# Performance work log

Hardware: AMD Instinct MI355X
Metric: run time of the kernel (lower is better)

## Reference

```python
import jax, jax.numpy as jnp
import numpy as np

N, B, D, Q = 32, 36, 2048, 1024  # batch, objects, v_dim, q_dim


def setup_inputs() -> dict:
    key = jax.random.key(0)
    ks = jax.random.split(key, 6)
    sc = 0.02  # small init so ReLU chains stay well-scaled
    return {
        "v": jax.random.normal(ks[0], (N, B, D), jnp.float32),
        "q": jax.random.normal(ks[1], (N, Q), jnp.float32),
        "W1": jax.random.normal(ks[2], (D, D), jnp.float32) * sc,
        "b1": jnp.zeros((D,), jnp.float32),
        "W2": jax.random.normal(ks[3], (D, D), jnp.float32) * sc,
        "b2": jnp.zeros((D,), jnp.float32),
        "W3": jax.random.normal(ks[4], (Q, D), jnp.float32) * sc,
        "b3": jnp.zeros((D,), jnp.float32),
    }


def reference(v, q, W1, b1, W2, b2, W3, b3):
    # FCNet = ReLU(Linear(.)) with weight-norm folded, dropout=0 (eval).
    # Original calls linear3 twice (linear4 unused bug), so q_emb == q_emb2.
    qe = jax.nn.relu(q @ W3 + b3)  # (N, D)
    # pairs[n,i,j] = v[n,i]*qe[n] + v[n,j]*qe[n]  -> (N, B, B, D)
    pairs = (v[:, :, None, :] + v[:, None, :, :]) * qe[:, None, None, :]
    h = jax.nn.relu(jnp.einsum('nijd,de->nije', pairs, W1) + b1)  # linear1
    x = jnp.sum(h, axis=2)  # sum over j relations -> (N, B, D)
    return jax.nn.relu(x @ W2 + b2)  # linear2
```

## Files before the change

kernel.cpp:

```cpp
#include <hip/hip_runtime.h>
#include <stdint.h>

#define N_BATCH 32
#define B_OBJ   36
#define D_DIM   2048
#define Q_DIM   1024

typedef __bf16 bf16x8 __attribute__((ext_vector_type(8)));
typedef float  f32x4  __attribute__((ext_vector_type(4)));

__device__ __forceinline__ uint16_t f2bf(float f) {
    uint32_t u = __builtin_bit_cast(uint32_t, f);
    uint32_t r = (u + 0x7FFFu + ((u >> 16) & 1u)) >> 16;
    return (uint16_t)r;
}

__device__ __forceinline__ void gld_lds16(const void* g, void* l) {
    __builtin_amdgcn_global_load_lds(
        (const __attribute__((address_space(1))) uint32_t*)g,
        (__attribute__((address_space(3))) uint32_t*)l, 16, 0, 0);
}

__global__ __launch_bounds__(256) void transpose_all(
    const float* __restrict__ W1, const float* __restrict__ W2,
    uint16_t* __restrict__ W1t, uint16_t* __restrict__ W2t) {
    __shared__ float tile[64][65];
    int gy = blockIdx.y;
    const float* W; uint16_t* Wt; int k0;
    if (gy < 32) { W = W1; Wt = W1t; k0 = gy * 64; }
    else         { W = W2; Wt = W2t; k0 = (gy - 32) * 64; }
    int n0 = blockIdx.x * 64;
    int t = threadIdx.x;
    {
        int r = t >> 4, c = (t & 15) * 4;
#pragma unroll
        for (int p = 0; p < 4; ++p)
            *(float4*)&tile[r + p * 16][c] =
                *(const float4*)&W[(size_t)(k0 + r + p * 16) * 2048 + n0 + c];
    }
    __syncthreads();
    {
        int n = t >> 2, kb = (t & 3) * 16;
#pragma unroll
        for (int g4 = 0; g4 < 4; ++g4) {
            int k = kb + g4 * 4;
            ushort4 o;
            o.x = f2bf(tile[k][n]);     o.y = f2bf(tile[k + 1][n]);
            o.z = f2bf(tile[k + 2][n]); o.w = f2bf(tile[k + 3][n]);
            *(ushort4*)&Wt[(size_t)(n0 + n) * 2048 + k0 + k] = o;
        }
    }
}

__global__ __launch_bounds__(256) void qe_f32(
    const float* __restrict__ q, const float* __restrict__ W3,
    float* __restrict__ qpart) {
    __shared__ float qs[128][32];
    int t = threadIdx.x;
    int e0 = blockIdx.x * 64;
    int kbase = blockIdx.y * 128;
    {
        int nn = t >> 3, kg = (t & 7) * 16;
#pragma unroll
        for (int p = 0; p < 4; ++p) {
            float4 f = *(const float4*)&q[(size_t)nn * Q_DIM + kbase + kg + p * 4];
            qs[kg + p * 4 + 0][nn] = f.x; qs[kg + p * 4 + 1][nn] = f.y;
            qs[kg + p * 4 + 2][nn] = f.z; qs[kg + p * 4 + 3][nn] = f.w;
        }
    }
    __syncthreads();
    int n = t >> 3, e8 = (t & 7) * 8;
    float acc[8] = {};
#pragma unroll 4
    for (int k = 0; k < 128; ++k) {
        float qv = qs[k][n];
        float4 wa = *(const float4*)&W3[(size_t)(kbase + k) * D_DIM + e0 + e8];
        float4 wb = *(const float4*)&W3[(size_t)(kbase + k) * D_DIM + e0 + e8 + 4];
        acc[0] += qv * wa.x; acc[1] += qv * wa.y; acc[2] += qv * wa.z; acc[3] += qv * wa.w;
        acc[4] += qv * wb.x; acc[5] += qv * wb.y; acc[6] += qv * wb.z; acc[7] += qv * wb.w;
    }
    float* dst = qpart + (size_t)blockIdx.y * 32 * D_DIM + (size_t)n * D_DIM + e0 + e8;
    *(float4*)dst = *(float4*)&acc[0];
    *(float4*)(dst + 4) = *(float4*)&acc[4];
}

__global__ __launch_bounds__(256) void qe_makeu(
    const float* __restrict__ qpart, const float* __restrict__ b3,
    const float* __restrict__ v, uint16_t* __restrict__ u) {
    int n = blockIdx.y;
    int c4 = blockIdx.x * 256 + threadIdx.x;
    const float4* p = (const float4*)qpart;
    size_t base = (size_t)n * 512 + c4;
    float4 s = p[base];
#pragma unroll
    for (int z = 1; z < 8; ++z) {
        float4 sz = p[(size_t)z * 16384 + base];
        s.x += sz.x; s.y += sz.y; s.z += sz.z; s.w += sz.w;
    }
    float4 b = ((const float4*)b3)[c4];
    float4 qe;
    qe.x = fmaxf(s.x + b.x, 0.f); qe.y = fmaxf(s.y + b.y, 0.f);
    qe.z = fmaxf(s.z + b.z, 0.f); qe.w = fmaxf(s.w + b.w, 0.f);
    const float4* v4 = (const float4*)v + (size_t)n * B_OBJ * 512 + c4;
    ushort4* u4 = (ushort4*)u + (size_t)n * B_OBJ * 512 + c4;
#pragma unroll 4
    for (int i = 0; i < B_OBJ; ++i) {
        float4 vv = v4[(size_t)i * 512];
        ushort4 o;
        o.x = f2bf(vv.x * qe.x); o.y = f2bf(vv.y * qe.y);
        o.z = f2bf(vv.z * qe.z); o.w = f2bf(vv.w * qe.w);
        u4[(size_t)i * 512] = o;
    }
}

__global__ __launch_bounds__(256) void gemm_ks(
    const uint16_t* __restrict__ A,
    const uint16_t* __restrict__ Bt,
    float* __restrict__ Yp) {
    __shared__ __align__(16) uint16_t sm[24576];
    int t = threadIdx.x, lane = t & 63, wave = t >> 6;
    int l15 = lane & 15, quad = lane >> 4;
    int wr = wave >> 1, wc = wave & 1;
    int n0 = blockIdx.x * 64, m0 = blockIdx.y * 128, kz = blockIdx.z;
    const uint16_t* Ab = A  + (size_t)m0 * D_DIM + kz * 1024;
    const uint16_t* Bb = Bt + (size_t)n0 * D_DIM + kz * 1024;

    const uint16_t* gp[6]; uint16_t* lp[6]; int ofs[6];
#pragma unroll
    for (int c = 0; c < 6; ++c) {
        int r = wave + 4 * c;
        int row16 = lane >> 2, kin = (lane & 3) * 8;
        if (r < 16) {
            int h = r >> 3, g = r & 7;
            gp[c] = Ab + (size_t)(g * 16 + row16) * D_DIM + h * 32 + kin;
            lp[c] = sm + h * 4096 + g * 512;
            ofs[c] = 8192;
        } else {
            int rb = r - 16, h = rb >> 2, g = rb & 3;
            gp[c] = Bb + (size_t)(g * 16 + row16) * D_DIM + h * 32 + kin;
            lp[c] = sm + 16384 + h * 2048 + g * 512;
            ofs[c] = 4096;
        }
    }

    f32x4 acc[4][2] = {};

#pragma unroll
    for (int c = 0; c < 6; ++c) gld_lds16(gp[c], lp[c]);

    for (int it = 0; it < 16; ++it) {
        int buf = it & 1;
        __syncthreads();
        if (it < 15) {
            int nxt = buf ^ 1;
#pragma unroll
            for (int c = 0; c < 6; ++c)
                gld_lds16(gp[c] + (it + 1) * 64, lp[c] + nxt * ofs[c]);
        }
#pragma unroll
        for (int s = 0; s < 2; ++s) {
            bf16x8 af[4], bfr[2];
#pragma unroll
            for (int i = 0; i < 4; ++i)
                af[i] = *(const bf16x8*)(sm + buf * 8192 + s * 4096 +
                                         (wr * 64 + i * 16 + l15) * 32 + quad * 8);
#pragma unroll
            for (int j = 0; j < 2; ++j)
                bfr[j] = *(const bf16x8*)(sm + 16384 + buf * 4096 + s * 2048 +
                                          (wc * 32 + j * 16 + l15) * 32 + quad * 8);
#pragma unroll
            for (int i = 0; i < 4; ++i)
#pragma unroll
                for (int j = 0; j < 2; ++j)
                    acc[i][j] = __builtin_amdgcn_mfma_f32_16x16x32_bf16(af[i], bfr[j], acc[i][j], 0, 0, 0);
        }
    }

    float* Y = Yp + (size_t)kz * 1152 * D_DIM;
#pragma unroll
    for (int i = 0; i < 4; ++i)
#pragma unroll
        for (int j = 0; j < 2; ++j) {
            int col = n0 + wc * 32 + j * 16 + l15;
#pragma unroll
            for (int r = 0; r < 4; ++r)
                Y[(size_t)(m0 + wr * 64 + i * 16 + quad * 4 + r) * D_DIM + col] = acc[i][j][r];
        }
}

__global__ __launch_bounds__(256) void pairsum_red(
    const float* __restrict__ Yp, const float* __restrict__ b1,
    uint16_t* __restrict__ X) {
    int n = blockIdx.y;
    int d = blockIdx.x * 256 + threadIdx.x;
    const float* y0 = Yp + (size_t)(n * B_OBJ) * D_DIM + d;
    const float* y1 = y0 + (size_t)1152 * D_DIM;
    float z[B_OBJ];
#pragma unroll
    for (int j = 0; j < B_OBJ; ++j)
        z[j] = y0[(size_t)j * D_DIM] + y1[(size_t)j * D_DIM];
    float b = b1[d];
    uint16_t* xb = X + (size_t)(n * B_OBJ) * D_DIM + d;
#pragma unroll
    for (int i = 0; i < B_OBJ; ++i) {
        float zi = z[i] + b;
        float s = 0.f;
#pragma unroll
        for (int j = 0; j < B_OBJ; ++j) s += fmaxf(zi + z[j], 0.f);
        xb[(size_t)i * D_DIM] = f2bf(s);
    }
}

__global__ __launch_bounds__(256) void reduce_out(
    const float* __restrict__ Op, const float* __restrict__ b2,
    float* __restrict__ out) {
    int i = blockIdx.x * 256 + threadIdx.x;
    const float4* p = (const float4*)Op;
    float4 a = p[i], b = p[589824 + i];
    float4 bb = ((const float4*)b2)[i & 511];
    float4 o;
    o.x = fmaxf(a.x + b.x + bb.x, 0.f);
    o.y = fmaxf(a.y + b.y + bb.y, 0.f);
    o.z = fmaxf(a.z + b.z + bb.z, 0.f);
    o.w = fmaxf(a.w + b.w + bb.w, 0.f);
    ((float4*)out)[i] = o;
}

extern "C" void kernel_launch(void* const* d_in, const int* in_sizes, int n_in,
                              void* d_out, int out_size, void* d_ws, size_t ws_size,
                              hipStream_t stream) {
    const float* v  = (const float*)d_in[0];
    const float* q  = (const float*)d_in[1];
    const float* W1 = (const float*)d_in[2];
    const float* b1 = (const float*)d_in[3];
    const float* W2 = (const float*)d_in[4];
    const float* b2 = (const float*)d_in[5];
    const float* W3 = (const float*)d_in[6];
    const float* b3 = (const float*)d_in[7];
    float* out = (float*)d_out;

    char* ws = (char*)d_ws;
    uint16_t* W1t   = (uint16_t*)(ws + 0);
    uint16_t* W2t   = (uint16_t*)(ws + 8388608);
    uint16_t* u     = (uint16_t*)(ws + 16777216);
    float*    qpart = (float*)   (ws + 21495808);
    uint16_t* x     = (uint16_t*)(ws + 23592960);
    float*    Yp    = (float*)   (ws + 28311552);
    float*    Op    = Yp;

    transpose_all<<<dim3(32, 64), 256, 0, stream>>>(W1, W2, W1t, W2t);

    qe_f32<<<dim3(32, 8), 256, 0, stream>>>(q, W3, qpart);
    qe_makeu<<<dim3(2, N_BATCH), 256, 0, stream>>>(qpart, b3, v, u);

    gemm_ks<<<dim3(32, 9, 2), 256, 0, stream>>>(u, W1t, Yp);
    pairsum_red<<<dim3(8, N_BATCH), 256, 0, stream>>>(Yp, b1, x);

    gemm_ks<<<dim3(32, 9, 2), 256, 0, stream>>>(x, W2t, Op);
    reduce_out<<<2304, 256, 0, stream>>>(Op, b2, out);
}
```

Before: 185.8 us.

## Fuse pairwise-relu reduction and bias epilogues into full-K GEMM with 32x32 MFMA

Result: slower. 190.3 us (+2.4%).

```diff
diff --git a/kernel.cpp b/kernel.cpp
--- a/kernel.cpp
+++ b/kernel.cpp
@@ -6,8 +6,9 @@
 #define D_DIM   2048
 #define Q_DIM   1024
 
-typedef __bf16 bf16x8 __attribute__((ext_vector_type(8)));
-typedef float  f32x4  __attribute__((ext_vector_type(4)));
+typedef __bf16 bf16x8  __attribute__((ext_vector_type(8)));
+typedef float  f32x4   __attribute__((ext_vector_type(4)));
+typedef float  f32x16  __attribute__((ext_vector_type(16)));
 
 __device__ __forceinline__ uint16_t f2bf(float f) {
     uint32_t u = __builtin_bit_cast(uint32_t, f);
@@ -113,117 +114,108 @@
     }
 }
 
-__global__ __launch_bounds__(256) void gemm_ks(
+__global__ __launch_bounds__(128) void gemm_fused(
     const uint16_t* __restrict__ A,
     const uint16_t* __restrict__ Bt,
-    float* __restrict__ Yp) {
-    __shared__ __align__(16) uint16_t sm[24576];
+    const float* __restrict__ bias,
+    void* __restrict__ Cv,
+    int mode) {
+    __shared__ __align__(16) uint16_t sm[20480];
+    float* yt = (float*)sm;
+
     int t = threadIdx.x, lane = t & 63, wave = t >> 6;
-    int l15 = lane & 15, quad = lane >> 4;
-    int wr = wave >> 1, wc = wave & 1;
-    int n0 = blockIdx.x * 64, m0 = blockIdx.y * 128, kz = blockIdx.z;
-    const uint16_t* Ab = A  + (size_t)m0 * D_DIM + kz * 1024;
-    const uint16_t* Bb = Bt + (size_t)n0 * D_DIM + kz * 1024;
-
-    const uint16_t* gp[6]; uint16_t* lp[6]; int ofs[6];
-#pragma unroll
-    for (int c = 0; c < 6; ++c) {
-        int r = wave + 4 * c;
+    int l31 = lane & 31, khalf = lane >> 5;
+    int bg = blockIdx.y;
+    int n0 = blockIdx.x * 64;
+    const uint16_t* Ab = A + (size_t)bg * 72 * D_DIM;
+
+    const uint16_t* gp[10]; uint16_t* lp[10]; int bufstep[10];
+    {
         int row16 = lane >> 2, kin = (lane & 3) * 8;
-        if (r < 16) {
-            int h = r >> 3, g = r & 7;
-            gp[c] = Ab + (size_t)(g * 16 + row16) * D_DIM + h * 32 + kin;
-            lp[c] = sm + h * 4096 + g * 512;
-            ofs[c] = 8192;
-        } else {
-            int rb = r - 16, h = rb >> 2, g = rb & 3;
-            gp[c] = Bb + (size_t)(g * 16 + row16) * D_DIM + h * 32 + kin;
-            lp[c] = sm + 16384 + h * 2048 + g * 512;
-            ofs[c] = 4096;
-        }
-    }
-
-    f32x4 acc[4][2] = {};
-
-#pragma unroll
-    for (int c = 0; c < 6; ++c) gld_lds16(gp[c], lp[c]);
-
-    for (int it = 0; it < 16; ++it) {
+#pragma unroll
+        for (int c = 0; c < 10; ++c) {
+            int r = wave * 10 + c;
+            if (r < 12) {
+                int h = r / 6, g = r % 6;
+                gp[c] = Ab + (size_t)(g * 16 + row16) * D_DIM + h * 32 + kin;
+                lp[c] = sm + h * 3072 + g * 512;
+                bufstep[c] = 6144;
+            } else {
+                int rb = r - 12, h = rb >> 2, g = rb & 3;
+                gp[c] = Bt + (size_t)(n0 + g * 16 + row16) * D_DIM + h * 32 + kin;
+                lp[c] = sm + 12288 + h * 2048 + g * 512;
+                bufstep[c] = 4096;
+            }
+        }
+    }
+
+    f32x16 acc[3] = {};
+
+#pragma unroll
+    for (int c = 0; c < 10; ++c) gld_lds16(gp[c], lp[c]);
+
+    for (int it = 0; it < 32; ++it) {
         int buf = it & 1;
         __syncthreads();
-        if (it < 15) {
+        if (it < 31) {
             int nxt = buf ^ 1;
 #pragma unroll
-            for (int c = 0; c < 6; ++c)
-                gld_lds16(gp[c] + (it + 1) * 64, lp[c] + nxt * ofs[c]);
-        }
-#pragma unroll
-        for (int s = 0; s < 2; ++s) {
-            bf16x8 af[4], bfr[2];
-#pragma unroll
-            for (int i = 0; i < 4; ++i)
-                af[i] = *(const bf16x8*)(sm + buf * 8192 + s * 4096 +
-                                         (wr * 64 + i * 16 + l15) * 32 + quad * 8);
-#pragma unroll
-            for (int j = 0; j < 2; ++j)
-                bfr[j] = *(const bf16x8*)(sm + 16384 + buf * 4096 + s * 2048 +
-                                          (wc * 32 + j * 16 + l15) * 32 + quad * 8);
-#pragma unroll
-            for (int i = 0; i < 4; ++i)
-#pragma unroll
-                for (int j = 0; j < 2; ++j)
-                    acc[i][j] = __builtin_amdgcn_mfma_f32_16x16x32_bf16(af[i], bfr[j], acc[i][j], 0, 0, 0);
-        }
-    }
-
-    float* Y = Yp + (size_t)kz * 1152 * D_DIM;
-#pragma unroll
-    for (int i = 0; i < 4; ++i)
-#pragma unroll
-        for (int j = 0; j < 2; ++j) {
-            int col = n0 + wc * 32 + j * 16 + l15;
-#pragma unroll
-            for (int r = 0; r < 4; ++r)
-                Y[(size_t)(m0 + wr * 64 + i * 16 + quad * 4 + r) * D_DIM + col] = acc[i][j][r];
-        }
-}
-
-__global__ __launch_bounds__(256) void pairsum_red(
-    const float* __restrict__ Yp, const float* __restrict__ b1,
-    uint16_t* __restrict__ X) {
-    int n = blockIdx.y;
-    int d = blockIdx.x * 256 + threadIdx.x;
-    const float* y0 = Yp + (size_t)(n * B_OBJ) * D_DIM + d;
-    const float* y1 = y0 + (size_t)1152 * D_DIM;
-    float z[B_OBJ];
-#pragma unroll
-    for (int j = 0; j < B_OBJ; ++j)
-        z[j] = y0[(size_t)j * D_DIM] + y1[(size_t)j * D_DIM];
-    float b = b1[d];
-    uint16_t* xb = X + (size_t)(n * B_OBJ) * D_DIM + d;
-#pragma unroll
-    for (int i = 0; i < B_OBJ; ++i) {
-        float zi = z[i] + b;
-        float s = 0.f;
-#pragma unroll
-        for (int j = 0; j < B_OBJ; ++j) s += fmaxf(zi + z[j], 0.f);
-        xb[(size_t)i * D_DIM] = f2bf(s);
-    }
-}
-
-__global__ __launch_bounds__(256) void reduce_out(
-    const float* __restrict__ Op, const float* __restrict__ b2,
-    float* __restrict__ out) {
-    int i = blockIdx.x * 256 + threadIdx.x;
-    const float4* p = (const float4*)Op;
-    float4 a = p[i], b = p[589824 + i];
-    float4 bb = ((const float4*)b2)[i & 511];
-    float4 o;
-    o.x = fmaxf(a.x + b.x + bb.x, 0.f);
-    o.y = fmaxf(a.y + b.y + bb.y, 0.f);
-    o.z = fmaxf(a.z + b.z + bb.z, 0.f);
-    o.w = fmaxf(a.w + b.w + bb.w, 0.f);
-    ((float4*)out)[i] = o;
+            for (int c = 0; c < 10; ++c)
+                gld_lds16(gp[c] + (size_t)(it + 1) * 64, lp[c] + nxt * bufstep[c]);
+        }
+#pragma unroll
+        for (int s = 0; s < 4; ++s) {
+            int h = s >> 1, kin = (s & 1) * 16 + khalf * 8;
+            bf16x8 bfr = *(const bf16x8*)(sm + 12288 + buf * 4096 + h * 2048 +
+                                          (wave * 32 + l31) * 32 + kin);
+#pragma unroll
+            for (int mt = 0; mt < 3; ++mt) {
+                bf16x8 af = *(const bf16x8*)(sm + buf * 6144 + h * 3072 +
+                                             (mt * 32 + l31) * 32 + kin);
+                acc[mt] = __builtin_amdgcn_mfma_f32_32x32x16_bf16(af, bfr, acc[mt], 0, 0, 0);
+            }
+        }
+    }
+
+    if (mode == 0) {
+        uint16_t* X = (uint16_t*)Cv;
+        __syncthreads();
+#pragma unroll
+        for (int mt = 0; mt < 3; ++mt)
+#pragma unroll
+            for (int reg = 0; reg < 16; ++reg) {
+                int row = mt * 32 + (reg & 3) + 8 * (reg >> 2) + 4 * khalf;
+                if (row < 72) yt[row * 68 + wave * 32 + l31] = acc[mt][reg];
+            }
+        __syncthreads();
+        int col = t & 63, half = t >> 6;
+        float b = bias[n0 + col];
+        float z[36];
+#pragma unroll
+        for (int j = 0; j < 36; ++j) z[j] = yt[(half * 36 + j) * 68 + col];
+        uint16_t* xb = X + (size_t)(bg * 72 + half * 36) * D_DIM + n0 + col;
+#pragma unroll
+        for (int i = 0; i < 36; ++i) {
+            float zi = z[i] + b;
+            float ssum = 0.f;
+#pragma unroll
+            for (int j = 0; j < 36; ++j) ssum += fmaxf(zi + z[j], 0.f);
+            xb[(size_t)i * D_DIM] = f2bf(ssum);
+        }
+    } else {
+        float* O = (float*)Cv;
+        int col = n0 + wave * 32 + l31;
+        float b = bias[col];
+#pragma unroll
+        for (int mt = 0; mt < 3; ++mt)
+#pragma unroll
+            for (int reg = 0; reg < 16; ++reg) {
+                int row = mt * 32 + (reg & 3) + 8 * (reg >> 2) + 4 * khalf;
+                if (row < 72)
+                    O[(size_t)(bg * 72 + row) * D_DIM + col] =
+                        fmaxf(acc[mt][reg] + b, 0.f);
+            }
+    }
 }
 
 extern "C" void kernel_launch(void* const* d_in, const int* in_sizes, int n_in,
@@ -245,17 +237,13 @@
     uint16_t* u     = (uint16_t*)(ws + 16777216);
     float*    qpart = (float*)   (ws + 21495808);
     uint16_t* x     = (uint16_t*)(ws + 23592960);
-    float*    Yp    = (float*)   (ws + 28311552);
-    float*    Op    = Yp;
 
     transpose_all<<<dim3(32, 64), 256, 0, stream>>>(W1, W2, W1t, W2t);
 
     qe_f32<<<dim3(32, 8), 256, 0, stream>>>(q, W3, qpart);
     qe_makeu<<<dim3(2, N_BATCH), 256, 0, stream>>>(qpart, b3, v, u);
 
-    gemm_ks<<<dim3(32, 9, 2), 256, 0, stream>>>(u, W1t, Yp);
-    pairsum_red<<<dim3(8, N_BATCH), 256, 0, stream>>>(Yp, b1, x);
-
-    gemm_ks<<<dim3(32, 9, 2), 256, 0, stream>>>(x, W2t, Op);
-    reduce_out<<<2304, 256, 0, stream>>>(Op, b2, out);
-}
+    gemm_fused<<<dim3(32, 16), 128, 0, stream>>>(u, W1t, b1, x, 0);
+
+    gemm_fused<<<dim3(32, 16), 128, 0, stream>>>(x, W2t, b2, out, 1);
+}
```
